# Kernel tuning notes

Hardware: AMD Instinct MI355X
Metric: run time of the kernel (lower is better)

Reference implementation:

```python
import jax, jax.numpy as jnp
import numpy as np

HW = 16            # hardcoded hw_seq_len in the module
THETA = 10000.0

def _rope_tables(head_dim):
    # EVA VisionRotaryEmbeddingFast: per-axis rope dim = head_dim // 2
    hd = head_dim // 2
    inv_freq = 1.0 / (THETA ** (np.arange(0, hd, 2, dtype=np.float32) / hd))  # (hd//2,)
    t = np.arange(HW, dtype=np.float32)                # ft_seq_len == pt_seq_len
    f = np.einsum('i,j->ij', t, inv_freq)              # (HW, hd//2)
    f = np.repeat(f, 2, axis=-1)                       # (HW, hd)
    fx = np.broadcast_to(f[:, None, :], (HW, HW, hd))  # vary along rows
    fy = np.broadcast_to(f[None, :, :], (HW, HW, hd))  # vary along cols
    F = np.concatenate([fx, fy], axis=-1).reshape(HW * HW, head_dim)  # (256, head_dim)
    return jnp.asarray(np.cos(F)), jnp.asarray(np.sin(F))

def _rotate_half(x):
    # '... (d r) -> ... d r' with r=2; (x1, x2) -> (-x2, x1)
    x = x.reshape(*x.shape[:-1], -1, 2)
    x1, x2 = x[..., 0], x[..., 1]
    return jnp.stack((-x2, x1), axis=-1).reshape(*x.shape[:-2], -1)

def setup_inputs() -> dict:
    key = jax.random.key(0)
    k1, k2, k3 = jax.random.split(key, 3)
    B, N, C = 64, 256, 1024
    x = jax.random.normal(k1, (B, N, C), dtype=jnp.float32)
    qkv_w = jax.random.normal(k2, (3 * C, C), dtype=jnp.float32) * (C ** -0.5)
    proj_w = jax.random.normal(k3, (C, C), dtype=jnp.float32) * (C ** -0.5)
    proj_b = jnp.zeros((C,), dtype=jnp.float32)
    return {"x": x, "qkv_w": qkv_w, "proj_w": proj_w, "proj_b": proj_b}

def reference(x, qkv_w, proj_w, proj_b):
    B, N, C = x.shape
    H = 16
    D = C // H
    cos, sin = _rope_tables(D)  # (N, D) each; constants
    qkv = jnp.einsum('bnc,oc->bno', x, qkv_w).reshape(B, N, 3, H, D)
    qkv = jnp.transpose(qkv, (2, 0, 3, 1, 4))  # (3, B, H, N, D)
    q, k, v = qkv[0], qkv[1], qkv[2]
    q = q * cos + _rotate_half(q) * sin
    k = k * cos + _rotate_half(k) * sin
    scale = D ** -0.5
    scores = jnp.einsum('bhnd,bhmd->bhnm', q, k) * scale
    attn = jax.nn.softmax(scores, axis=-1)
    out = jnp.einsum('bhnm,bhmd->bhnd', attn, v)
    out = jnp.transpose(out, (0, 2, 1, 3)).reshape(B, N, C)
    return jnp.einsum('bnc,oc->bno', out, proj_w) + proj_b
```

## Files before the change

kernel.cpp:

```cpp
#include <hip/hip_runtime.h>
#include <stdint.h>

typedef __attribute__((ext_vector_type(8))) short bf16x8;
typedef __attribute__((ext_vector_type(4))) short bf16x4;
typedef __attribute__((ext_vector_type(4))) float f32x4;
typedef __attribute__((ext_vector_type(4))) unsigned short u16x4;

typedef __attribute__((address_space(3))) unsigned short lds_u16;
typedef const __attribute__((address_space(1))) unsigned short glb_u16;

__device__ __forceinline__ unsigned short f2bf(float f) {
  union { float f; unsigned u; } x; x.f = f;
  unsigned r = x.u + 0x7FFFu + ((x.u >> 16) & 1u);
  return (unsigned short)(r >> 16);
}

__global__ __launch_bounds__(256) void k_cvt(const float* __restrict__ in,
                                             unsigned short* __restrict__ out, int n4) {
  int i = blockIdx.x * 256 + threadIdx.x;
  if (i >= n4) return;
  f32x4 v = reinterpret_cast<const f32x4*>(in)[i];
  u16x4 o;
  o[0] = f2bf(v[0]); o[1] = f2bf(v[1]); o[2] = f2bf(v[2]); o[3] = f2bf(v[3]);
  reinterpret_cast<u16x4*>(out)[i] = o;
}

__global__ void k_tables(float* __restrict__ cosT, float* __restrict__ sinT) {
  int n = threadIdx.x;
  int r = n >> 4, cc = n & 15;
  for (int d = 0; d < 64; ++d) {
    int tpos = (d < 32) ? r : cc;
    int j = (d & 31) >> 1;
    float ang = (float)tpos * powf(10000.0f, -(float)j * (1.0f / 16.0f));
    cosT[n * 64 + d] = cosf(ang);
    sinT[n * 64 + d] = sinf(ang);
  }
}

template <int EPI>
__global__ __launch_bounds__(512, 2) void k_gemm(
    const unsigned short* __restrict__ A,
    const unsigned short* __restrict__ B,
    int M, int N, int K, int nTM,
    const float* __restrict__ cosT, const float* __restrict__ sinT,
    unsigned short* __restrict__ qout, unsigned short* __restrict__ kout,
    unsigned short* __restrict__ vTout,
    const float* __restrict__ bias, float* __restrict__ fout) {
  __shared__ unsigned short smem_u16[65536];

  const int t = threadIdx.x, w = t >> 6, l = t & 63, c = l & 15, g = l >> 4;
  const int wm = w >> 2, wn = w & 3;

  const int nwg = gridDim.x;
  const int bid = (int)blockIdx.x;
  const int nTN = nwg / nTM;
  const int xcd = bid & 7;
  const int j = bid >> 3;
  const int tn = j % nTN;
  const int tm = xcd * (nTM >> 3) + j / nTN;
  const int m0 = tm * 256, n0 = tn * 256;

  const int rS = t >> 3;
  const int colS = ((t & 7) * 8) ^ (((t >> 5) & 1) << 4);
  const unsigned short* Asrc = A + (size_t)(m0 + rS) * K + colS;
  const unsigned short* Bsrc = B + (size_t)(n0 + rS) * K + colS;
  const size_t hK = (size_t)128 * K;
  const size_t iK = (size_t)64 * K;

#define STG_A(db, half, i, kt)                                                              \
  __builtin_amdgcn_global_load_lds((glb_u16*)(Asrc + (half) * hK + (i) * iK + (kt) * 64),   \
      (lds_u16*)&smem_u16[((db) * 32768 + (half) * 16384 + (i) * 8192 + w * 1024) >> 1],    \
      16, 0, 0)
#define STG_B(db, half, i, kt)                                                                      \
  __builtin_amdgcn_global_load_lds((glb_u16*)(Bsrc + (half) * hK + (i) * iK + (kt) * 64),           \
      (lds_u16*)&smem_u16[(65536 + (db) * 32768 + (half) * 16384 + (i) * 8192 + w * 1024) >> 1],    \
      16, 0, 0)

#pragma unroll
  for (int kk = 0; kk < 2; ++kk) {
    STG_A(kk, 0, 0, kk); STG_A(kk, 0, 1, kk); STG_A(kk, 1, 0, kk); STG_A(kk, 1, 1, kk);
    STG_B(kk, 0, 0, kk); STG_B(kk, 0, 1, kk); STG_B(kk, 1, 0, kk); STG_B(kk, 1, 1, kk);
  }

  f32x4 acc[8][4];
#pragma unroll
  for (int i = 0; i < 8; ++i)
#pragma unroll
    for (int jj = 0; jj < 4; ++jj) acc[i][jj] = 0.0f;

  const int xm = ((c >> 2) & 1) << 5;
  const int ko0 = (g * 16) ^ xm;
  const int ko1 = ko0 + 64;
  const int rAb = (wm * 128 + c) * 128;
  const int rBb = (wn * 64 + c) * 128;

  asm volatile("s_waitcnt vmcnt(8)" ::: "memory");
  __builtin_amdgcn_s_barrier();
  asm volatile("" ::: "memory");

  bf16x8 a0[4][2], a1[4][2], bq[4][2];
  const int nKT = K >> 6;
  for (int k = 0; k < nKT; ++k) {
    const int db = k & 1;
    const int Abo = db * 32768;
    const int Bbo = 65536 + db * 32768;
    const int k2 = k + 2;
    const bool st = (k2 < nKT);

#pragma unroll
    for (int mf = 0; mf < 4; ++mf) {
      a0[mf][0] = *(const bf16x8*)&smem_u16[(Abo + rAb + mf * 2048 + ko0) >> 1];
      a0[mf][1] = *(const bf16x8*)&smem_u16[(Abo + rAb + mf * 2048 + ko1) >> 1];
    }
#pragma unroll
    for (int nf = 0; nf < 4; ++nf) {
      bq[nf][0] = *(const bf16x8*)&smem_u16[(Bbo + rBb + nf * 2048 + ko0) >> 1];
      bq[nf][1] = *(const bf16x8*)&smem_u16[(Bbo + rBb + nf * 2048 + ko1) >> 1];
    }
#pragma unroll
    for (int mf = 0; mf < 4; ++mf) {
      a1[mf][0] = *(const bf16x8*)&smem_u16[(Abo + rAb + (mf + 4) * 2048 + ko0) >> 1];
      a1[mf][1] = *(const bf16x8*)&smem_u16[(Abo + rAb + (mf + 4) * 2048 + ko1) >> 1];
    }
    asm volatile("s_waitcnt lgkmcnt(8)" ::: "memory");
    __builtin_amdgcn_sched_barrier(0);
    __builtin_amdgcn_s_setprio(1);
#pragma unroll
    for (int mf = 0; mf < 4; ++mf)
#pragma unroll
      for (int nf = 0; nf < 2; ++nf)
#pragma unroll
        for (int ks = 0; ks < 2; ++ks)
          acc[mf][nf] = __builtin_amdgcn_mfma_f32_16x16x32_bf16(a0[mf][ks], bq[nf][ks], acc[mf][nf], 0, 0, 0);
    __builtin_amdgcn_s_setprio(0);
    asm volatile("s_waitcnt lgkmcnt(0)" ::: "memory");
    __builtin_amdgcn_sched_barrier(0);
    __builtin_amdgcn_s_barrier();
    asm volatile("" ::: "memory");

    if (st) { STG_A(db, 0, 0, k2); STG_A(db, 1, 0, k2); STG_B(db, 0, 0, k2); }
    __builtin_amdgcn_s_setprio(1);
#pragma unroll
    for (int mf = 0; mf < 4; ++mf)
#pragma unroll
      for (int nf = 2; nf < 4; ++nf)
#pragma unroll
        for (int ks = 0; ks < 2; ++ks)
          acc[mf][nf] = __builtin_amdgcn_mfma_f32_16x16x32_bf16(a0[mf][ks], bq[nf][ks], acc[mf][nf], 0, 0, 0);
    __builtin_amdgcn_s_setprio(0);
    __builtin_amdgcn_sched_barrier(0);
    __builtin_amdgcn_s_barrier();
    asm volatile("" ::: "memory");

    if (st) { STG_A(db, 0, 1, k2); STG_A(db, 1, 1, k2); STG_B(db, 0, 1, k2); }
    __builtin_amdgcn_s_setprio(1);
#pragma unroll
    for (int mf = 0; mf < 4; ++mf)
#pragma unroll
      for (int nf = 0; nf < 2; ++nf)
#pragma unroll
        for (int ks = 0; ks < 2; ++ks)
          acc[mf + 4][nf] = __builtin_amdgcn_mfma_f32_16x16x32_bf16(a1[mf][ks], bq[nf][ks], acc[mf + 4][nf], 0, 0, 0);
    __builtin_amdgcn_s_setprio(0);
    __builtin_amdgcn_sched_barrier(0);
    __builtin_amdgcn_s_barrier();
    asm volatile("" ::: "memory");

    if (st) { STG_B(db, 1, 0, k2); STG_B(db, 1, 1, k2); }
    __builtin_amdgcn_s_setprio(1);
#pragma unroll
    for (int mf = 0; mf < 4; ++mf)
#pragma unroll
      for (int nf = 2; nf < 4; ++nf)
#pragma unroll
        for (int ks = 0; ks < 2; ++ks)
          acc[mf + 4][nf] = __builtin_amdgcn_mfma_f32_16x16x32_bf16(a1[mf][ks], bq[nf][ks], acc[mf + 4][nf], 0, 0, 0);
    __builtin_amdgcn_s_setprio(0);
    __builtin_amdgcn_sched_barrier(0);
    if (k < nKT - 2) {
      asm volatile("s_waitcnt vmcnt(8)" ::: "memory");
      __builtin_amdgcn_s_barrier();
      asm volatile("" ::: "memory");
    } else if (k == nKT - 2) {
      asm volatile("s_waitcnt vmcnt(0)" ::: "memory");
      __builtin_amdgcn_s_barrier();
      asm volatile("" ::: "memory");
    }
  }
#undef STG_A
#undef STG_B

  if constexpr (EPI == 0) {
    const int which = n0 >> 10;
    unsigned short* qk = (which == 0) ? qout : kout;
#pragma unroll
    for (int nf = 0; nf < 4; ++nf) {
      const int o = n0 + wn * 64 + nf * 16 + c;
      const int h = (o >> 6) & 15;
      const int d = o & 63;
      if (which < 2) {
        const float sgn = (d & 1) ? 1.0f : -1.0f;
        const float qscale = (which == 0) ? 0.125f : 1.0f;
#pragma unroll
        for (int mf = 0; mf < 8; ++mf) {
          const int m = m0 + wm * 128 + mf * 16 + g * 4;
          const int bb = m >> 8;
          const int nb = m & 255;
          f32x4 v = acc[mf][nf];
          f32x4 p;
          p[0] = __shfl_xor(v[0], 1);
          p[1] = __shfl_xor(v[1], 1);
          p[2] = __shfl_xor(v[2], 1);
          p[3] = __shfl_xor(v[3], 1);
          size_t base = ((size_t)(bb * 16 + h) * 256 + nb) * 64 + d;
#pragma unroll
          for (int jj = 0; jj < 4; ++jj) {
            const int n = nb + jj;
            const float cv = cosT[n * 64 + d];
            const float sv = sinT[n * 64 + d];
            float ov = (v[jj] * cv + sgn * p[jj] * sv) * qscale;
            qk[base + (size_t)jj * 64] = f2bf(ov);
          }
        }
      } else {
#pragma unroll
        for (int mf = 0; mf < 8; ++mf) {
          const int m = m0 + wm * 128 + mf * 16 + g * 4;
          const int bb = m >> 8;
          const int nb = m & 255;
          f32x4 v = acc[mf][nf];
          u16x4 pk;
          pk[0] = f2bf(v[0]); pk[1] = f2bf(v[1]); pk[2] = f2bf(v[2]); pk[3] = f2bf(v[3]);
          size_t idx = ((size_t)(bb * 16 + h) * 64 + d) * 256 + nb;
          *reinterpret_cast<u16x4*>(vTout + idx) = pk;
        }
      }
    }
  } else {
#pragma unroll
    for (int nf = 0; nf < 4; ++nf) {
      const int o = n0 + wn * 64 + nf * 16 + c;
      const float bv = bias[o];
#pragma unroll
      for (int mf = 0; mf < 8; ++mf) {
        const int m = m0 + wm * 128 + mf * 16 + g * 4;
        f32x4 v = acc[mf][nf];
#pragma unroll
        for (int jj = 0; jj < 4; ++jj) fout[(size_t)(m + jj) * N + o] = v[jj] + bv;
      }
    }
  }
}

__global__ __launch_bounds__(256) void k_attn(const unsigned short* __restrict__ Q,
                                              const unsigned short* __restrict__ Kb,
                                              const unsigned short* __restrict__ VT,
                                              unsigned short* __restrict__ Out) {
  constexpr int LDK = 80, LDP = 80;
  __shared__ unsigned short klds[64 * LDK];
  __shared__ unsigned short plds[4][64 * LDP];
  const int bh = blockIdx.x;
  const int bb = bh >> 4, h = bh & 15;
  const int t = threadIdx.x, w = t >> 6, l = t & 63, c = l & 15, g = l >> 4;
  const unsigned short* qh = Q + (size_t)bh * 256 * 64;
  const unsigned short* kh = Kb + (size_t)bh * 256 * 64;
  const unsigned short* vh = VT + (size_t)bh * 64 * 256;
  const int q0 = w * 64;

  bf16x8 qf[4][2];
#pragma unroll
  for (int nf = 0; nf < 4; ++nf)
#pragma unroll
    for (int ks = 0; ks < 2; ++ks)
      qf[nf][ks] = *reinterpret_cast<const bf16x8*>(qh + (q0 + nf * 16 + c) * 64 + ks * 32 + g * 8);

  f32x4 oacc[4][4];
#pragma unroll
  for (int i = 0; i < 4; ++i)
#pragma unroll
    for (int jj = 0; jj < 4; ++jj) oacc[i][jj] = 0.0f;
  float mr[4] = {-1e30f, -1e30f, -1e30f, -1e30f};
  float lr[4] = {0.f, 0.f, 0.f, 0.f};

  for (int ch = 0; ch < 4; ++ch) {
    __syncthreads();
    {
      int row = t >> 3, col = (t & 7) * 8;
#pragma unroll
      for (int rep = 0; rep < 2; ++rep) {
        int r = rep * 32 + row;
        bf16x8 kv = *reinterpret_cast<const bf16x8*>(kh + (ch * 64 + r) * 64 + col);
        *reinterpret_cast<bf16x8*>(&klds[r * LDK + col]) = kv;
      }
    }
    __syncthreads();

    f32x4 s[4][4];
#pragma unroll
    for (int i = 0; i < 4; ++i)
#pragma unroll
      for (int jj = 0; jj < 4; ++jj) s[i][jj] = 0.0f;
#pragma unroll
    for (int ks = 0; ks < 2; ++ks) {
      bf16x8 kf[4];
#pragma unroll
      for (int mf = 0; mf < 4; ++mf)
        kf[mf] = *reinterpret_cast<const bf16x8*>(&klds[(mf * 16 + c) * LDK + ks * 32 + g * 8]);
#pragma unroll
      for (int mf = 0; mf < 4; ++mf)
#pragma unroll
        for (int nf = 0; nf < 4; ++nf)
          s[mf][nf] = __builtin_amdgcn_mfma_f32_16x16x32_bf16(kf[mf], qf[nf][ks], s[mf][nf], 0, 0, 0);
    }

#pragma unroll
    for (int nf = 0; nf < 4; ++nf) {
      float mx = -1e30f;
#pragma unroll
      for (int mf = 0; mf < 4; ++mf)
#pragma unroll
        for (int jj = 0; jj < 4; ++jj) mx = fmaxf(mx, s[mf][nf][jj]);
      mx = fmaxf(mx, __shfl_xor(mx, 16));
      mx = fmaxf(mx, __shfl_xor(mx, 32));
      float mnew = fmaxf(mr[nf], mx);
      float rsc = __expf(mr[nf] - mnew);
      mr[nf] = mnew;
      float sum = 0.f;
#pragma unroll
      for (int mf = 0; mf < 4; ++mf)
#pragma unroll
        for (int jj = 0; jj < 4; ++jj) {
          float p = __expf(s[mf][nf][jj] - mnew);
          s[mf][nf][jj] = p;
          sum += p;
        }
      sum += __shfl_xor(sum, 16);
      sum += __shfl_xor(sum, 32);
      lr[nf] = lr[nf] * rsc + sum;
#pragma unroll
      for (int mf = 0; mf < 4; ++mf) oacc[mf][nf] *= rsc;
    }

#pragma unroll
    for (int mf = 0; mf < 4; ++mf)
#pragma unroll
      for (int nf = 0; nf < 4; ++nf) {
        bf16x4 pk;
        pk[0] = (short)f2bf(s[mf][nf][0]);
        pk[1] = (short)f2bf(s[mf][nf][1]);
        pk[2] = (short)f2bf(s[mf][nf][2]);
        pk[3] = (short)f2bf(s[mf][nf][3]);
        *reinterpret_cast<bf16x4*>(&plds[w][(nf * 16 + c) * LDP + mf * 16 + g * 4]) = pk;
      }

#pragma unroll
    for (int ks = 0; ks < 2; ++ks) {
      bf16x8 vf[4], pf[4];
#pragma unroll
      for (int mf = 0; mf < 4; ++mf)
        vf[mf] = *reinterpret_cast<const bf16x8*>(vh + (mf * 16 + c) * 256 + ch * 64 + ks * 32 + g * 8);
#pragma unroll
      for (int nf = 0; nf < 4; ++nf) {
        bf16x4 p0 = *reinterpret_cast<const bf16x4*>(&plds[w][(nf * 16 + c) * LDP + ks * 32 + g * 8]);
        bf16x4 p1 = *reinterpret_cast<const bf16x4*>(&plds[w][(nf * 16 + c) * LDP + ks * 32 + g * 8 + 4]);
        pf[nf] = __builtin_shufflevector(p0, p1, 0, 1, 2, 3, 4, 5, 6, 7);
      }
#pragma unroll
      for (int mf = 0; mf < 4; ++mf)
#pragma unroll
        for (int nf = 0; nf < 4; ++nf)
          oacc[mf][nf] = __builtin_amdgcn_mfma_f32_16x16x32_bf16(vf[mf], pf[nf], oacc[mf][nf], 0, 0, 0);
    }
  }

  float linv[4];
#pragma unroll
  for (int nf = 0; nf < 4; ++nf) linv[nf] = 1.0f / lr[nf];
#pragma unroll
  for (int mf = 0; mf < 4; ++mf)
#pragma unroll
    for (int nf = 0; nf < 4; ++nf) {
      f32x4 v = oacc[mf][nf];
      u16x4 pk;
      pk[0] = f2bf(v[0] * linv[nf]);
      pk[1] = f2bf(v[1] * linv[nf]);
      pk[2] = f2bf(v[2] * linv[nf]);
      pk[3] = f2bf(v[3] * linv[nf]);
      size_t row = (size_t)bb * 256 + q0 + nf * 16 + c;
      size_t idx = row * 1024 + (size_t)h * 64 + mf * 16 + g * 4;
      *reinterpret_cast<u16x4*>(Out + idx) = pk;
    }
}

extern "C" void kernel_launch(void* const* d_in, const int* in_sizes, int n_in,
                              void* d_out, int out_size, void* d_ws, size_t ws_size,
                              hipStream_t stream) {
  const float* x = (const float*)d_in[0];
  const float* wqkv = (const float*)d_in[1];
  const float* wproj = (const float*)d_in[2];
  const float* bproj = (const float*)d_in[3];

  char* ws = (char*)d_ws;
  unsigned short* xb = (unsigned short*)(ws);
  unsigned short* wqkvb = (unsigned short*)(ws + 33554432);
  unsigned short* wprojb = (unsigned short*)(ws + 39845888);
  float* cosT = (float*)(ws + 41943040);
  float* sinT = (float*)(ws + 42008576);
  unsigned short* qb = (unsigned short*)(ws + 42074112);
  unsigned short* kb = (unsigned short*)(ws + 75628544);
  unsigned short* vtb = (unsigned short*)(ws + 109182976);
  unsigned short* attn_out = xb;

  k_cvt<<<16384, 256, 0, stream>>>(x, xb, 4194304);
  k_cvt<<<3072, 256, 0, stream>>>(wqkv, wqkvb, 786432);
  k_cvt<<<1024, 256, 0, stream>>>(wproj, wprojb, 262144);
  k_tables<<<1, 256, 0, stream>>>(cosT, sinT);

  k_gemm<0><<<64 * 12, 512, 0, stream>>>(xb, wqkvb, 16384, 3072, 1024, 64,
                                         cosT, sinT, qb, kb, vtb, nullptr, nullptr);
  k_attn<<<1024, 256, 0, stream>>>(qb, kb, vtb, attn_out);
  k_gemm<1><<<64 * 4, 512, 0, stream>>>(attn_out, wprojb, 16384, 1024, 1024, 64,
                                        nullptr, nullptr, nullptr, nullptr, nullptr,
                                        bproj, (float*)d_out);
}
```

Measured before the change: 299.0 us.

## Software-pipeline LDS fragment reads across MFMA quarters and prefetch next tile

```diff
diff --git a/kernel.cpp b/kernel.cpp
--- a/kernel.cpp
+++ b/kernel.cpp
@@ -94,101 +94,93 @@
   const int rAb = (wm * 128 + c) * 128;
   const int rBb = (wn * 64 + c) * 128;
 
+  bf16x8 a0[4][2], a1[4][2], bq[4][2];
+
+#define RD_A0(Abo)                                                                       \
+  _Pragma("unroll") for (int mf = 0; mf < 4; ++mf) {                                     \
+    a0[mf][0] = *(const bf16x8*)&smem_u16[((Abo) + rAb + mf * 2048 + ko0) >> 1];         \
+    a0[mf][1] = *(const bf16x8*)&smem_u16[((Abo) + rAb + mf * 2048 + ko1) >> 1];         \
+  }
+#define RD_A1(Abo)                                                                       \
+  _Pragma("unroll") for (int mf = 0; mf < 4; ++mf) {                                     \
+    a1[mf][0] = *(const bf16x8*)&smem_u16[((Abo) + rAb + (mf + 4) * 2048 + ko0) >> 1];   \
+    a1[mf][1] = *(const bf16x8*)&smem_u16[((Abo) + rAb + (mf + 4) * 2048 + ko1) >> 1];   \
+  }
+#define RD_BLO(Bbo)                                                                      \
+  _Pragma("unroll") for (int nf = 0; nf < 2; ++nf) {                                     \
+    bq[nf][0] = *(const bf16x8*)&smem_u16[((Bbo) + rBb + nf * 2048 + ko0) >> 1];         \
+    bq[nf][1] = *(const bf16x8*)&smem_u16[((Bbo) + rBb + nf * 2048 + ko1) >> 1];         \
+  }
+#define RD_BHI(Bbo)                                                                      \
+  _Pragma("unroll") for (int nf = 2; nf < 4; ++nf) {                                     \
+    bq[nf][0] = *(const bf16x8*)&smem_u16[((Bbo) + rBb + nf * 2048 + ko0) >> 1];         \
+    bq[nf][1] = *(const bf16x8*)&smem_u16[((Bbo) + rBb + nf * 2048 + ko1) >> 1];         \
+  }
+#define MFMA_Q(am, bl, bh, mo)                                                           \
+  __builtin_amdgcn_s_setprio(1);                                                         \
+  _Pragma("unroll") for (int mf = 0; mf < 4; ++mf)                                       \
+  _Pragma("unroll") for (int nf = (bl); nf < (bh); ++nf)                                 \
+  _Pragma("unroll") for (int ks = 0; ks < 2; ++ks)                                       \
+      acc[mf + (mo)][nf] =                                                               \
+          __builtin_amdgcn_mfma_f32_16x16x32_bf16(am[mf][ks], bq[nf][ks], acc[mf + (mo)][nf], 0, 0, 0); \
+  __builtin_amdgcn_s_setprio(0);                                                         \
+  __builtin_amdgcn_sched_barrier(0)
+
   asm volatile("s_waitcnt vmcnt(8)" ::: "memory");
   __builtin_amdgcn_s_barrier();
   asm volatile("" ::: "memory");
-
-  bf16x8 a0[4][2], a1[4][2], bq[4][2];
+  RD_A0(0);
+  RD_BLO(65536);
+
   const int nKT = K >> 6;
   for (int k = 0; k < nKT; ++k) {
     const int db = k & 1;
     const int Abo = db * 32768;
     const int Bbo = 65536 + db * 32768;
+    const int nAbo = (db ^ 1) * 32768;
+    const int nBbo = 65536 + (db ^ 1) * 32768;
     const int k2 = k + 2;
     const bool st = (k2 < nKT);
 
-#pragma unroll
-    for (int mf = 0; mf < 4; ++mf) {
-      a0[mf][0] = *(const bf16x8*)&smem_u16[(Abo + rAb + mf * 2048 + ko0) >> 1];
-      a0[mf][1] = *(const bf16x8*)&smem_u16[(Abo + rAb + mf * 2048 + ko1) >> 1];
-    }
-#pragma unroll
-    for (int nf = 0; nf < 4; ++nf) {
-      bq[nf][0] = *(const bf16x8*)&smem_u16[(Bbo + rBb + nf * 2048 + ko0) >> 1];
-      bq[nf][1] = *(const bf16x8*)&smem_u16[(Bbo + rBb + nf * 2048 + ko1) >> 1];
-    }
-#pragma unroll
-    for (int mf = 0; mf < 4; ++mf) {
-      a1[mf][0] = *(const bf16x8*)&smem_u16[(Abo + rAb + (mf + 4) * 2048 + ko0) >> 1];
-      a1[mf][1] = *(const bf16x8*)&smem_u16[(Abo + rAb + (mf + 4) * 2048 + ko1) >> 1];
-    }
-    asm volatile("s_waitcnt lgkmcnt(8)" ::: "memory");
-    __builtin_amdgcn_sched_barrier(0);
-    __builtin_amdgcn_s_setprio(1);
-#pragma unroll
-    for (int mf = 0; mf < 4; ++mf)
-#pragma unroll
-      for (int nf = 0; nf < 2; ++nf)
-#pragma unroll
-        for (int ks = 0; ks < 2; ++ks)
-          acc[mf][nf] = __builtin_amdgcn_mfma_f32_16x16x32_bf16(a0[mf][ks], bq[nf][ks], acc[mf][nf], 0, 0, 0);
-    __builtin_amdgcn_s_setprio(0);
     asm volatile("s_waitcnt lgkmcnt(0)" ::: "memory");
-    __builtin_amdgcn_sched_barrier(0);
+    RD_BHI(Bbo);
+    MFMA_Q(a0, 0, 2, 0);
     __builtin_amdgcn_s_barrier();
     asm volatile("" ::: "memory");
 
-    if (st) { STG_A(db, 0, 0, k2); STG_A(db, 1, 0, k2); STG_B(db, 0, 0, k2); }
-    __builtin_amdgcn_s_setprio(1);
-#pragma unroll
-    for (int mf = 0; mf < 4; ++mf)
-#pragma unroll
-      for (int nf = 2; nf < 4; ++nf)
-#pragma unroll
-        for (int ks = 0; ks < 2; ++ks)
-          acc[mf][nf] = __builtin_amdgcn_mfma_f32_16x16x32_bf16(a0[mf][ks], bq[nf][ks], acc[mf][nf], 0, 0, 0);
-    __builtin_amdgcn_s_setprio(0);
-    __builtin_amdgcn_sched_barrier(0);
+    RD_A1(Abo);
+    asm volatile("s_waitcnt lgkmcnt(8)" ::: "memory");
+    if (st) { STG_A(db, 0, 0, k2); STG_A(db, 1, 0, k2); }
+    MFMA_Q(a0, 2, 4, 0);
     __builtin_amdgcn_s_barrier();
     asm volatile("" ::: "memory");
 
-    if (st) { STG_A(db, 0, 1, k2); STG_A(db, 1, 1, k2); STG_B(db, 0, 1, k2); }
-    __builtin_amdgcn_s_setprio(1);
-#pragma unroll
-    for (int mf = 0; mf < 4; ++mf)
-#pragma unroll
-      for (int nf = 0; nf < 2; ++nf)
-#pragma unroll
-        for (int ks = 0; ks < 2; ++ks)
-          acc[mf + 4][nf] = __builtin_amdgcn_mfma_f32_16x16x32_bf16(a1[mf][ks], bq[nf][ks], acc[mf + 4][nf], 0, 0, 0);
-    __builtin_amdgcn_s_setprio(0);
-    __builtin_amdgcn_sched_barrier(0);
+    asm volatile("s_waitcnt lgkmcnt(0)" ::: "memory");
+    if (st) { STG_B(db, 0, 0, k2); STG_B(db, 0, 1, k2); STG_B(db, 1, 0, k2); STG_B(db, 1, 1, k2); }
+    MFMA_Q(a1, 0, 2, 4);
     __builtin_amdgcn_s_barrier();
     asm volatile("" ::: "memory");
 
-    if (st) { STG_B(db, 1, 0, k2); STG_B(db, 1, 1, k2); }
-    __builtin_amdgcn_s_setprio(1);
-#pragma unroll
-    for (int mf = 0; mf < 4; ++mf)
-#pragma unroll
-      for (int nf = 2; nf < 4; ++nf)
-#pragma unroll
-        for (int ks = 0; ks < 2; ++ks)
-          acc[mf + 4][nf] = __builtin_amdgcn_mfma_f32_16x16x32_bf16(a1[mf][ks], bq[nf][ks], acc[mf + 4][nf], 0, 0, 0);
-    __builtin_amdgcn_s_setprio(0);
-    __builtin_amdgcn_sched_barrier(0);
+    if (st) { STG_A(db, 0, 1, k2); STG_A(db, 1, 1, k2); }
     if (k < nKT - 2) {
       asm volatile("s_waitcnt vmcnt(8)" ::: "memory");
-      __builtin_amdgcn_s_barrier();
-      asm volatile("" ::: "memory");
     } else if (k == nKT - 2) {
       asm volatile("s_waitcnt vmcnt(0)" ::: "memory");
-      __builtin_amdgcn_s_barrier();
-      asm volatile("" ::: "memory");
-    }
+    }
+    __builtin_amdgcn_s_barrier();
+    asm volatile("" ::: "memory");
+    if (k + 1 < nKT) { RD_A0(nAbo); RD_BLO(nBbo); }
+    MFMA_Q(a1, 2, 4, 4);
+    __builtin_amdgcn_s_barrier();
+    asm volatile("" ::: "memory");
   }
 #undef STG_A
 #undef STG_B
+#undef RD_A0
+#undef RD_A1
+#undef RD_BLO
+#undef RD_BHI
+#undef MFMA_Q
 
   if constexpr (EPI == 0) {
     const int which = n0 >> 10;
```

Result: faster. 286.0 us (-4.4%).
